# Performance work log

Measured on AMD Instinct MI355X. Metric: run time of the kernel, lower is better.

The kernel has to match this reference:

```python
import jax, jax.numpy as jnp
import numpy as np

V = 30000
Y = 30000
D = 768
B = 8
N = 512
PAD_ID = 0
POS_EXPONENT = 1
NEG_INF = 1e12
LN_EPS = 1e-5


def setup_inputs() -> dict:
    key = jax.random.key(0)
    k1, k2, k3, k4, k5 = jax.random.split(key, 5)
    M_s = jax.random.randint(k1, (B, N), 0, V, dtype=jnp.int64)
    E_v = jax.random.normal(k2, (V, D), dtype=jnp.float32) * 0.02
    E_y = jax.random.normal(k3, (Y, D), dtype=jnp.float32) * 0.02
    # padding_idx=0 -> zero rows
    E_v = E_v.at[PAD_ID].set(0.0)
    E_y = E_y.at[PAD_ID].set(0.0)
    W_A = jax.random.normal(k4, (D, D), dtype=jnp.float32) * (1.0 / np.sqrt(D))
    W_O = jax.random.normal(k5, (D, D), dtype=jnp.float32) * (1.0 / np.sqrt(D))
    gamma = jnp.ones((D,), dtype=jnp.float32)
    beta = jnp.zeros((D,), dtype=jnp.float32)
    return {"M_s": M_s, "E_v": E_v, "E_y": E_y, "W_A": W_A, "W_O": W_O,
            "gamma": gamma, "beta": beta}


def positional_rep(seq_len: int, exponent: int) -> jnp.ndarray:
    idx = jnp.arange(seq_len)
    rel = (idx[None, :] - idx[:, None]).astype(jnp.float32)  # [N, N], j - i
    sign = jnp.where(rel >= 0, 1.0, -1.0)
    return sign * jnp.abs(rel) ** exponent


def layer_norm(x, gamma, beta):
    mu = jnp.mean(x, axis=-1, keepdims=True)
    var = jnp.mean((x - mu) ** 2, axis=-1, keepdims=True)
    return (x - mu) * jax.lax.rsqrt(var + LN_EPS) * gamma + beta


def reference(M_s, E_v, E_y, W_A, W_O, gamma, beta):
    # Embedding lookup (dropout is identity at eval / p=0)
    X = E_v[M_s]                                   # [B, N, D]
    Q = X                                          # self-attention mode (v_q=None)
    mask = (M_s != PAD_ID)                         # [B, N]

    # attention: logits = (Q @ W_A) @ X^T + pos_bias, mask, softmax
    logits = jnp.einsum('bnd,bmd->bnm', Q @ W_A, X)  # [B, N, N]
    logits = logits + positional_rep(X.shape[1], POS_EXPONENT)[None]
    logits = jnp.where(mask[:, None, :], logits, -NEG_INF)
    A = jax.nn.softmax(logits, axis=-1)            # [B, N, N]
    Q_c = jnp.einsum('bnm,bmd->bnd', A, X @ W_O)   # [B, N, D]

    H = layer_norm(Q_c + Q, gamma, beta)           # [B, N, D]
    y_logits = jnp.einsum('bnd,yd->bny', H, E_y)   # [B, N, Y]
    return y_logits, A
```

## Files before the change

kernel.cpp:

```cpp
#include <hip/hip_runtime.h>
#include <hip/hip_bf16.h>

using bf16 = __hip_bfloat16;
typedef __attribute__((ext_vector_type(8))) short bf16x8;
typedef __attribute__((ext_vector_type(4))) float f32x4;

#define DEV __device__ __forceinline__

#define AS1 __attribute__((address_space(1)))
#define AS3 __attribute__((address_space(3)))
#define SB  __builtin_amdgcn_sched_barrier(0)
#define BARR __builtin_amdgcn_s_barrier()
#define LG0 asm volatile("s_waitcnt lgkmcnt(0)" ::: "memory")
#define VM3 asm volatile("s_waitcnt vmcnt(3)" ::: "memory")
#define VM1 asm volatile("s_waitcnt vmcnt(1)" ::: "memory")
#define VM0 asm volatile("s_waitcnt vmcnt(0)" ::: "memory")

static constexpr int Bsz = 8, Nseq = 512, Dm = 768, Vv = 30000, Yv = 30000;
static constexpr int Ypad = 30208;
static constexpr int Tok = Bsz * Nseq;
static constexpr int NT = Dm / 32;

__global__ __launch_bounds__(512, 4)
void gemm_big(const bf16* __restrict__ Ag, const bf16* __restrict__ Bg,
              float* __restrict__ Cg)
{
    __shared__ bf16 sm[6][4096];

    int bid = blockIdx.x;
    { int cpx = gridDim.x >> 3; bid = (bid & 7) * cpx + (bid >> 3); }
    const int mT = bid & 31;
    const int nT = bid >> 5;

    const int tid  = threadIdx.x;
    const int lane = tid & 63;
    const int wid  = tid >> 6;
    const int wm   = wid >> 2;
    const int wn   = wid & 3;

    const int lr = tid >> 2;
    const int sc = ((tid & 3) ^ (lr & 3)) << 3;
    const bf16* aS  = Ag + (long)(mT * 128 + lr) * Dm + sc;
    const bf16* bS0 = Bg + (long)(nT * 256 + lr) * Dm + sc;
    const bf16* bS1 = bS0 + (long)128 * Dm;
    const int ldsW = wid << 9;

    const int fl = lane & 15;
    const int fh = lane >> 4;
    const int e0 = (fh ^ (fl & 3)) << 3;
    const int aro = (wm * 64 + fl) * 32;
    const int bro = (wn * 32 + fl) * 32;

    bf16x8 afr[4], bfr[2];
    f32x4 acc[4][2][2] = {};

#define STG(CI, PTR, T)                                                        \
    __builtin_amdgcn_global_load_lds((const AS1 void*)((PTR) + (T) * 32),      \
        (AS3 void*)&sm[CI][ldsW], 16, 0, 0);
#define RA(CI)                                                                 \
    _Pragma("unroll") for (int mm = 0; mm < 4; ++mm)                           \
        afr[mm] = *(const bf16x8*)&sm[CI][aro + mm * 512 + e0];
#define RB(CI)                                                                 \
    _Pragma("unroll") for (int nn = 0; nn < 2; ++nn)                           \
        bfr[nn] = *(const bf16x8*)&sm[CI][bro + nn * 512 + e0];
#define MF8(NQ)                                                                \
    __builtin_amdgcn_s_setprio(1);                                             \
    _Pragma("unroll") for (int mm = 0; mm < 4; ++mm)                           \
    _Pragma("unroll") for (int nn = 0; nn < 2; ++nn)                           \
        acc[mm][NQ][nn] = __builtin_amdgcn_mfma_f32_16x16x32_bf16(             \
            afr[mm], bfr[nn], acc[mm][NQ][nn], 0, 0, 0);                       \
    __builtin_amdgcn_s_setprio(0);

    STG(0, aS, 0) STG(1, bS0, 0) STG(2, bS1, 0) STG(3, aS, 1) STG(4, bS0, 1)
    VM3; SB; BARR; SB;

#pragma unroll 1
    for (int t = 0; t < NT - 2; t += 2) {
        RA(0) RB(1)
        STG(5, bS1, t + 1)
        VM3; SB; BARR; LG0; SB;
        MF8(0)
        SB; BARR; SB;
        RB(2)
        STG(0, aS, t + 2) STG(1, bS0, t + 2)
        VM3; SB; BARR; LG0; SB;
        MF8(1)
        SB; BARR; SB;
        RA(3) RB(4)
        STG(2, bS1, t + 2)
        VM3; SB; BARR; LG0; SB;
        MF8(0)
        SB; BARR; SB;
        RB(5)
        STG(3, aS, t + 3) STG(4, bS0, t + 3)
        VM3; SB; BARR; LG0; SB;
        MF8(1)
        SB; BARR; SB;
    }

    {
        RA(0) RB(1)
        STG(5, bS1, NT - 1)
        VM3; SB; BARR; LG0; SB;
        MF8(0)
        SB; BARR; SB;
        RB(2)
        VM1; SB; BARR; LG0; SB;
        MF8(1)
        SB; BARR; SB;
        RA(3) RB(4)
        VM0; SB; BARR; LG0; SB;
        MF8(0)
        SB; BARR; SB;
        RB(5)
        SB; BARR; LG0; SB;
        MF8(1)
    }

    const int rB = mT * 128 + wm * 64 + fh * 4;
    const int cB = nT * 256 + wn * 32 + fl;
#pragma unroll
    for (int mm = 0; mm < 4; ++mm)
#pragma unroll
    for (int nq = 0; nq < 2; ++nq)
#pragma unroll
    for (int nn = 0; nn < 2; ++nn) {
        const int c = cB + nq * 128 + nn * 16;
        if (c >= Yv) continue;
        const int r = rB + mm * 16;
#pragma unroll
        for (int j = 0; j < 4; ++j)
            __builtin_nontemporal_store(acc[mm][nq][nn][j],
                                        Cg + (long)(r + j) * Yv + c);
    }
#undef STG
#undef RA
#undef RB
#undef MF8
}

template<bool STORE_BF16>
DEV void gemm_core(bf16* __restrict__ smem,
                   const bf16* __restrict__ A, const bf16* __restrict__ Bm,
                   void* __restrict__ Cg, int bid, int M, int K,
                   int lda, int ldb, int ldc)
{
    bf16* As = smem;
    bf16* Bs = smem + 128 * 32;

    const int nTilesM = M >> 7;
    const int mTile = bid % nTilesM;
    const int nTile = bid / nTilesM;

    const int tid  = threadIdx.x;
    const int wave = tid >> 6;
    const int lane = tid & 63;

    const int sRow = (wave << 4) + (lane >> 2);
    const int sCol = (lane & 3) << 3;

    const long aBase = (long)(mTile * 128) * lda;
    const long bBase = (long)(nTile * 128) * ldb;

    const int fl = lane & 15;
    const int fh = lane >> 4;
    const int wRow = (wave >> 1) << 6;
    const int wCol = (wave & 1) << 6;

    f32x4 acc[4][4] = {};

    for (int k0 = 0; k0 < K; k0 += 32) {
#pragma unroll
        for (int t = 0; t < 2; ++t) {
            const bf16* gA = A  + aBase + (long)(t * 64 + sRow) * lda + (k0 + sCol);
            const bf16* gB = Bm + bBase + (long)(t * 64 + sRow) * ldb + (k0 + sCol);
            bf16* lA = &As[(t * 64 + (wave << 4)) * 32];
            bf16* lB = &Bs[(t * 64 + (wave << 4)) * 32];
            __builtin_amdgcn_global_load_lds(
                (const AS1 void*)gA, (AS3 void*)lA, 16, 0, 0);
            __builtin_amdgcn_global_load_lds(
                (const AS1 void*)gB, (AS3 void*)lB, 16, 0, 0);
        }
        __syncthreads();

        bf16x8 af[4], bfg[4];
#pragma unroll
        for (int m = 0; m < 4; ++m)
            af[m] = *(const bf16x8*)&As[(wRow + m * 16 + fl) * 32 + fh * 8];
#pragma unroll
        for (int n = 0; n < 4; ++n)
            bfg[n] = *(const bf16x8*)&Bs[(wCol + n * 16 + fl) * 32 + fh * 8];
#pragma unroll
        for (int m = 0; m < 4; ++m)
#pragma unroll
            for (int n = 0; n < 4; ++n)
                acc[m][n] = __builtin_amdgcn_mfma_f32_16x16x32_bf16(
                    af[m], bfg[n], acc[m][n], 0, 0, 0);
        __syncthreads();
    }

    const int rBase = mTile * 128 + wRow + fh * 4;
    const int cBase = nTile * 128 + wCol + fl;
#pragma unroll
    for (int m = 0; m < 4; ++m) {
#pragma unroll
        for (int n = 0; n < 4; ++n) {
            int gc = cBase + n * 16;
            int gr = rBase + m * 16;
            if (STORE_BF16) {
                bf16* C = (bf16*)Cg;
#pragma unroll
                for (int j = 0; j < 4; ++j)
                    C[(long)(gr + j) * ldc + gc] = __float2bfloat16(acc[m][n][j]);
            } else {
                float* C = (float*)Cg;
#pragma unroll
                for (int j = 0; j < 4; ++j)
                    C[(long)(gr + j) * ldc + gc] = acc[m][n][j];
            }
        }
    }
}

template<bool STORE_BF16>
__global__ __launch_bounds__(256)
void gemm_bt(const bf16* __restrict__ Ag, const bf16* __restrict__ Bg,
             void* __restrict__ Cg, int M, int K,
             int lda, int ldb, int ldc, long sA, long sB, long sC)
{
    __shared__ bf16 smem[128 * 32 * 2];
    const int bz = blockIdx.z;
    char* C = (char*)Cg + (long)bz * sC * (STORE_BF16 ? 2 : 4);
    gemm_core<STORE_BF16>(smem, Ag + (long)bz * sA, Bg + (long)bz * sB,
                          (void*)C, blockIdx.x, M, K, lda, ldb, ldc);
}

__global__ __launch_bounds__(256)
void gemm_dual(const bf16* __restrict__ Xb, const bf16* __restrict__ Wcat,
               bf16* __restrict__ QWb, bf16* __restrict__ XWoT)
{
    __shared__ bf16 smem[128 * 32 * 2];
    const int bid = blockIdx.x;
    if (bid < 192)
        gemm_core<true>(smem, Xb, Wcat, (void*)QWb, bid, Tok, Dm, Dm, Dm, Dm);
    else
        gemm_core<true>(smem, Wcat + (size_t)Dm * Dm, Xb, (void*)XWoT,
                        bid - 192, Dm, Dm, Dm, Dm, Tok);
}

__global__ __launch_bounds__(256)
void gemm_bt64(const bf16* __restrict__ Ag, const bf16* __restrict__ Bg,
               bf16* __restrict__ Cg, int M, int K, int lda, int ldc,
               long sA, long sB, long sC)
{
    __shared__ bf16 As[64 * 32];
    __shared__ bf16 Bs[128 * 32];

    const int bz = blockIdx.z;
    const bf16* A  = Ag + (long)bz * sA;
    const bf16* Bm = Bg + (long)bz * sB;
    bf16* C = Cg + (long)bz * sC;

    const int bid = blockIdx.x;
    const int nTilesM = M >> 6;
    const int mTile = bid % nTilesM;
    const int nTile = bid / nTilesM;

    const int tid  = threadIdx.x;
    const int wave = tid >> 6;
    const int lane = tid & 63;

    const int sRow = tid >> 2;
    const int sCol = (tid & 3) << 3;

    const long aBase = (long)(mTile * 64) * lda;
    const long bBase = (long)(nTile * 128) * K;

    const int fl = lane & 15;
    const int fh = lane >> 4;

    f32x4 acc[4][2] = {};

    for (int k0 = 0; k0 < K; k0 += 32) {
        __builtin_amdgcn_global_load_lds(
            (const AS1 void*)(A + aBase + (long)sRow * lda + (k0 + sCol)),
            (AS3 void*)&As[wave * 512], 16, 0, 0);
#pragma unroll
        for (int t = 0; t < 2; ++t)
            __builtin_amdgcn_global_load_lds(
                (const AS1 void*)(Bm + bBase + (long)(t * 64 + sRow) * K + (k0 + sCol)),
                (AS3 void*)&Bs[t * 2048 + wave * 512], 16, 0, 0);
        __syncthreads();

        bf16x8 af[4], bfg[2];
#pragma unroll
        for (int m = 0; m < 4; ++m)
            af[m] = *(const bf16x8*)&As[(m * 16 + fl) * 32 + fh * 8];
#pragma unroll
        for (int n = 0; n < 2; ++n)
            bfg[n] = *(const bf16x8*)&Bs[(wave * 32 + n * 16 + fl) * 32 + fh * 8];
#pragma unroll
        for (int m = 0; m < 4; ++m)
#pragma unroll
            for (int n = 0; n < 2; ++n)
                acc[m][n] = __builtin_amdgcn_mfma_f32_16x16x32_bf16(
                    af[m], bfg[n], acc[m][n], 0, 0, 0);
        __syncthreads();
    }

    const int rBase = mTile * 64 + fh * 4;
    const int cBase = nTile * 128 + wave * 32 + fl;
#pragma unroll
    for (int m = 0; m < 4; ++m)
#pragma unroll
    for (int n = 0; n < 2; ++n) {
        const int gc = cBase + n * 16;
        const int gr = rBase + m * 16;
#pragma unroll
        for (int j = 0; j < 4; ++j)
            C[(long)(gr + j) * ldc + gc] = __float2bfloat16(acc[m][n][j]);
    }
}

static constexpr int PREP_CVT = 11328, PREP_WT = 1152, PREP_GATHER = 4096;

__global__ __launch_bounds__(256)
void k_prep(const float* __restrict__ Ey, bf16* __restrict__ Eyb,
            const float* __restrict__ WA, const float* __restrict__ WO,
            bf16* __restrict__ Wcat,
            const int* __restrict__ Ms, const float* __restrict__ Ev,
            bf16* __restrict__ Xb)
{
    __shared__ float t[32][33];
    const int b = blockIdx.x;
    const int tid = threadIdx.x;

    if (b < PREP_CVT) {
        const long idx = ((long)b * 256 + tid) * 8;
        const int row = (int)(idx / Dm);
        union { bf16 h[8]; uint4 u; } pk;
        if (row < Yv) {
            const f32x4* s = (const f32x4*)(Ey + idx);
            f32x4 a = __builtin_nontemporal_load(s);
            f32x4 c = __builtin_nontemporal_load(s + 1);
#pragma unroll
            for (int i = 0; i < 4; ++i) {
                pk.h[i]     = __float2bfloat16(a[i]);
                pk.h[4 + i] = __float2bfloat16(c[i]);
            }
        } else {
#pragma unroll
            for (int i = 0; i < 8; ++i) pk.h[i] = __float2bfloat16(0.f);
        }
        *(uint4*)(Eyb + idx) = pk.u;
    } else if (b < PREP_CVT + PREP_WT) {
        const int rem = b - PREP_CVT;
        const int z = rem / 576, r2 = rem % 576;
        const int bx = (r2 % 24) * 32, by = (r2 / 24) * 32;
        const float* W = z ? WO : WA;
        bf16* WT = Wcat + (size_t)z * Dm * Dm;
        const int tx = tid & 31, ty = tid >> 5;
#pragma unroll
        for (int i = 0; i < 32; i += 8)
            t[ty + i][tx] = W[(long)(bx + ty + i) * Dm + (by + tx)];
        __syncthreads();
#pragma unroll
        for (int i = 0; i < 32; i += 8)
            WT[(long)(by + ty + i) * Dm + (bx + tx)] = __float2bfloat16(t[tx][ty + i]);
    } else {
        const int token = b - (PREP_CVT + PREP_WT);
        if (tid < 192) {
            const int id = Ms[token];
            const int d = tid * 4;
            float4 v = *(const float4*)(Ev + (long)id * Dm + d);
            union { bf16 h[4]; uint2 u; } pk;
            pk.h[0] = __float2bfloat16(v.x); pk.h[1] = __float2bfloat16(v.y);
            pk.h[2] = __float2bfloat16(v.z); pk.h[3] = __float2bfloat16(v.w);
            *(uint2*)(Xb + (long)token * Dm + d) = pk.u;
        }
    }
}

DEV float waveMax(float v) {
#pragma unroll
    for (int o = 32; o > 0; o >>= 1) v = fmaxf(v, __shfl_xor(v, o, 64));
    return v;
}
DEV float waveSum(float v) {
#pragma unroll
    for (int o = 32; o > 0; o >>= 1) v += __shfl_xor(v, o, 64);
    return v;
}

__global__ __launch_bounds__(256) void k_softmax(const bf16* __restrict__ L,
                                                 const int* __restrict__ Ms,
                                                 float* __restrict__ Aout,
                                                 bf16* __restrict__ Ab)
{
    __shared__ float red[8];
    int row = blockIdx.x;
    int b = row >> 9, i = row & 511;
    const bf16* l = L + (long)row * Nseq;
    const int* ms = Ms + (b << 9);
    int t = threadIdx.x;
    int wid = t >> 6, lane = t & 63;
    int j0 = t, j1 = t + 256;

    float a0 = __bfloat162float(l[j0]) + (float)(j0 - i);
    float a1 = __bfloat162float(l[j1]) + (float)(j1 - i);
    if (ms[j0] == 0) a0 = -1e12f;
    if (ms[j1] == 0) a1 = -1e12f;

    float m = waveMax(fmaxf(a0, a1));
    if (lane == 0) red[wid] = m;
    __syncthreads();
    m = fmaxf(fmaxf(red[0], red[1]), fmaxf(red[2], red[3]));

    float e0 = expf(a0 - m), e1 = expf(a1 - m);
    float s = waveSum(e0 + e1);
    if (lane == 0) red[4 + wid] = s;
    __syncthreads();
    s = red[4] + red[5] + red[6] + red[7];
    float inv = 1.0f / s;

    float r0 = e0 * inv, r1 = e1 * inv;
    __builtin_nontemporal_store(r0, &Aout[(long)row * Nseq + j0]);
    __builtin_nontemporal_store(r1, &Aout[(long)row * Nseq + j1]);
    Ab[(long)row * Nseq + j0] = __float2bfloat16(r0);
    Ab[(long)row * Nseq + j1] = __float2bfloat16(r1);
}

__global__ __launch_bounds__(256) void k_ln(const bf16* __restrict__ Qc,
                                            const bf16* __restrict__ Xb,
                                            const float* __restrict__ gamma,
                                            const float* __restrict__ beta,
                                            bf16* __restrict__ Hb)
{
    __shared__ float red[8];
    int row = blockIdx.x;
    const bf16* q = Qc + (long)row * Dm;
    const bf16* e = Xb + (long)row * Dm;
    int t = threadIdx.x;
    int wid = t >> 6, lane = t & 63;

    float x[3];
#pragma unroll
    for (int c = 0; c < 3; ++c)
        x[c] = __bfloat162float(q[t + c * 256]) + __bfloat162float(e[t + c * 256]);

    float s = waveSum(x[0] + x[1] + x[2]);
    if (lane == 0) red[wid] = s;
    __syncthreads();
    float mu = (red[0] + red[1] + red[2] + red[3]) * (1.0f / 768.0f);

    float vs = 0.f;
#pragma unroll
    for (int c = 0; c < 3; ++c) { float d = x[c] - mu; vs += d * d; }
    vs = waveSum(vs);
    if (lane == 0) red[4 + wid] = vs;
    __syncthreads();
    float var = (red[4] + red[5] + red[6] + red[7]) * (1.0f / 768.0f);
    float rstd = rsqrtf(var + 1e-5f);

#pragma unroll
    for (int c = 0; c < 3; ++c) {
        int d = t + c * 256;
        Hb[(long)row * Dm + d] =
            __float2bfloat16((x[c] - mu) * rstd * gamma[d] + beta[d]);
    }
}

extern "C" void kernel_launch(void* const* d_in, const int* in_sizes, int n_in,
                              void* d_out, int out_size, void* d_ws, size_t ws_size,
                              hipStream_t stream)
{
    const int*   Ms    = (const int*)d_in[0];
    const float* Ev    = (const float*)d_in[1];
    const float* Ey    = (const float*)d_in[2];
    const float* WA    = (const float*)d_in[3];
    const float* WO    = (const float*)d_in[4];
    const float* gamma = (const float*)d_in[5];
    const float* beta  = (const float*)d_in[6];

    float* y_out = (float*)d_out;
    float* A_out = y_out + (size_t)Tok * Yv;

    char* ws = (char*)d_ws;
    size_t off = 0;
    auto alloc = [&](size_t n) { char* p = ws + off; off += (n + 255) & ~(size_t)255; return p; };
    bf16*  Xb    = (bf16*) alloc((size_t)Tok * Dm * 2);
    bf16*  WcatT = (bf16*) alloc((size_t)2 * Dm * Dm * 2);
    bf16*  QWb   = (bf16*) alloc((size_t)Tok * Dm * 2);
    bf16*  XWoT  = (bf16*) alloc((size_t)Dm * Tok * 2);
    bf16*  Lb    = (bf16*) alloc((size_t)Tok * Nseq * 2);
    bf16*  Ab    = (bf16*) alloc((size_t)Tok * Nseq * 2);
    bf16*  Qcb   = (bf16*) alloc((size_t)Tok * Dm * 2);
    bf16*  Hb    = (bf16*) alloc((size_t)Tok * Dm * 2);
    bf16*  Eyb   = (bf16*) alloc((size_t)Ypad * Dm * 2);

    k_prep<<<dim3(PREP_CVT + PREP_WT + PREP_GATHER), dim3(256), 0, stream>>>(
        Ey, Eyb, WA, WO, WcatT, Ms, Ev, Xb);
    gemm_dual<<<dim3(384), dim3(256), 0, stream>>>(Xb, WcatT, QWb, XWoT);
    gemm_bt64<<<dim3(32, 1, 8), dim3(256), 0, stream>>>(
        QWb, Xb, Lb, Nseq, Dm, Dm, Nseq,
        (long)Nseq * Dm, (long)Nseq * Dm, (long)Nseq * Nseq);
    k_softmax<<<dim3(Tok), dim3(256), 0, stream>>>(Lb, Ms, A_out, Ab);
    gemm_bt<true><<<dim3(24, 1, 8), dim3(256), 0, stream>>>(
        Ab, XWoT, (void*)Qcb, Nseq, Nseq, Nseq, Tok, Dm,
        (long)Nseq * Nseq, (long)Nseq, (long)Nseq * Dm);
    k_ln<<<dim3(Tok), dim3(256), 0, stream>>>(Qcb, Xb, gamma, beta, Hb);
    gemm_big<<<dim3(32 * (Ypad / 256)), dim3(512), 0, stream>>>(Hb, Eyb, y_out);
}
```

Measured before the change: 343.2 us.

## Restructure big GEMM pipeline into three-stage ring of full K-tile groups

The output-projection GEMM's LDS ring goes from six half-stage buffers to nine buffers, arranged as three groups of A, B0 and B1 K-tiles. Each phase now loads one full group and issues all 16 MFMAs per barrier pair, instead of 8 MFMAs with a staggered schedule of partial loads. The aim is fewer barriers per K step and more prefetch depth (two groups in flight). In exchange, LDS use per block rises from 48KB to 72KB and more B fragment registers are live, which may reduce occupancy against the launch bounds of 4.

```diff
diff --git a/kernel.cpp b/kernel.cpp
--- a/kernel.cpp
+++ b/kernel.cpp
@@ -13,7 +13,6 @@
 #define BARR __builtin_amdgcn_s_barrier()
 #define LG0 asm volatile("s_waitcnt lgkmcnt(0)" ::: "memory")
 #define VM3 asm volatile("s_waitcnt vmcnt(3)" ::: "memory")
-#define VM1 asm volatile("s_waitcnt vmcnt(1)" ::: "memory")
 #define VM0 asm volatile("s_waitcnt vmcnt(0)" ::: "memory")
 
 static constexpr int Bsz = 8, Nseq = 512, Dm = 768, Vv = 30000, Yv = 30000;
@@ -25,7 +24,7 @@
 void gemm_big(const bf16* __restrict__ Ag, const bf16* __restrict__ Bg,
               float* __restrict__ Cg)
 {
-    __shared__ bf16 sm[6][4096];
+    __shared__ bf16 sm[9][4096];
 
     int bid = blockIdx.x;
     { int cpx = gridDim.x >> 3; bid = (bid & 7) * cpx + (bid >> 3); }
@@ -51,70 +50,68 @@
     const int aro = (wm * 64 + fl) * 32;
     const int bro = (wn * 32 + fl) * 32;
 
-    bf16x8 afr[4], bfr[2];
+    bf16x8 afr[4], b0r[2], b1r[2];
     f32x4 acc[4][2][2] = {};
 
 #define STG(CI, PTR, T)                                                        \
     __builtin_amdgcn_global_load_lds((const AS1 void*)((PTR) + (T) * 32),      \
         (AS3 void*)&sm[CI][ldsW], 16, 0, 0);
+#define STGG(G, T)                                                             \
+    STG(3*(G) + 0, aS,  T) STG(3*(G) + 1, bS0, T) STG(3*(G) + 2, bS1, T)
 #define RA(CI)                                                                 \
     _Pragma("unroll") for (int mm = 0; mm < 4; ++mm)                           \
         afr[mm] = *(const bf16x8*)&sm[CI][aro + mm * 512 + e0];
-#define RB(CI)                                                                 \
+#define RB(BR, CI)                                                             \
     _Pragma("unroll") for (int nn = 0; nn < 2; ++nn)                           \
-        bfr[nn] = *(const bf16x8*)&sm[CI][bro + nn * 512 + e0];
-#define MF8(NQ)                                                                \
+        BR[nn] = *(const bf16x8*)&sm[CI][bro + nn * 512 + e0];
+#define RG(G)  RA(3*(G)) RB(b0r, 3*(G)+1) RB(b1r, 3*(G)+2)
+#define MF16                                                                   \
     __builtin_amdgcn_s_setprio(1);                                             \
     _Pragma("unroll") for (int mm = 0; mm < 4; ++mm)                           \
     _Pragma("unroll") for (int nn = 0; nn < 2; ++nn)                           \
-        acc[mm][NQ][nn] = __builtin_amdgcn_mfma_f32_16x16x32_bf16(             \
-            afr[mm], bfr[nn], acc[mm][NQ][nn], 0, 0, 0);                       \
+        acc[mm][0][nn] = __builtin_amdgcn_mfma_f32_16x16x32_bf16(              \
+            afr[mm], b0r[nn], acc[mm][0][nn], 0, 0, 0);                        \
+    _Pragma("unroll") for (int mm = 0; mm < 4; ++mm)                           \
+    _Pragma("unroll") for (int nn = 0; nn < 2; ++nn)                           \
+        acc[mm][1][nn] = __builtin_amdgcn_mfma_f32_16x16x32_bf16(              \
+            afr[mm], b1r[nn], acc[mm][1][nn], 0, 0, 0);                        \
     __builtin_amdgcn_s_setprio(0);
 
-    STG(0, aS, 0) STG(1, bS0, 0) STG(2, bS1, 0) STG(3, aS, 1) STG(4, bS0, 1)
+    STGG(0, 0) STGG(1, 1)
     VM3; SB; BARR; SB;
 
 #pragma unroll 1
-    for (int t = 0; t < NT - 2; t += 2) {
-        RA(0) RB(1)
-        STG(5, bS1, t + 1)
+    for (int t = 0; t < NT - 3; t += 3) {
+        RG(0)
+        STGG(2, t + 2)
         VM3; SB; BARR; LG0; SB;
-        MF8(0)
+        MF16
         SB; BARR; SB;
-        RB(2)
-        STG(0, aS, t + 2) STG(1, bS0, t + 2)
+        RG(1)
+        STGG(0, t + 3)
         VM3; SB; BARR; LG0; SB;
-        MF8(1)
+        MF16
         SB; BARR; SB;
-        RA(3) RB(4)
-        STG(2, bS1, t + 2)
+        RG(2)
+        STGG(1, t + 4)
         VM3; SB; BARR; LG0; SB;
-        MF8(0)
+        MF16
         SB; BARR; SB;
-        RB(5)
-        STG(3, aS, t + 3) STG(4, bS0, t + 3)
+    }
+
+    {
+        RG(0)
+        STGG(2, NT - 1)
         VM3; SB; BARR; LG0; SB;
-        MF8(1)
+        MF16
         SB; BARR; SB;
-    }
-
-    {
-        RA(0) RB(1)
-        STG(5, bS1, NT - 1)
-        VM3; SB; BARR; LG0; SB;
-        MF8(0)
+        RG(1)
+        VM0; SB; BARR; LG0; SB;
+        MF16
         SB; BARR; SB;
-        RB(2)
-        VM1; SB; BARR; LG0; SB;
-        MF8(1)
-        SB; BARR; SB;
-        RA(3) RB(4)
-        VM0; SB; BARR; LG0; SB;
-        MF8(0)
-        SB; BARR; SB;
-        RB(5)
-        SB; BARR; LG0; SB;
-        MF8(1)
+        RG(2)
+        SB; LG0; SB;
+        MF16
     }
 
     const int rB = mT * 128 + wm * 64 + fh * 4;
@@ -134,9 +131,11 @@
                                         Cg + (long)(r + j) * Yv + c);
     }
 #undef STG
+#undef STGG
 #undef RA
 #undef RB
-#undef MF8
+#undef RG
+#undef MF16
 }
 
 template<bool STORE_BF16>
```

New measurement: 339.5 us, median of 2. Within noise of the previous version (-1.1%).
